# Optimization experiments

Hardware: AMD Instinct MI355X
Metric: run time of the kernel (lower is better)

The kernel has to match this reference:

```python
import jax, jax.numpy as jnp
import numpy as np

DIM = 1024
NUM_HEADS = 16
HEAD_DIM = DIM // NUM_HEADS


def _slopes(num_heads):
    ratio = 2.0 ** (-8.0 / num_heads)
    return jnp.asarray([ratio ** i for i in range(1, num_heads + 1)], dtype=jnp.float32)


def setup_inputs() -> dict:
    key = jax.random.key(0)
    ks = jax.random.split(key, 10)
    b, q_len, k_len = 2, 2048, 4096
    query = jax.random.normal(ks[0], (b, q_len, DIM), dtype=jnp.float32)
    keys = jax.random.normal(ks[1], (b, k_len, DIM), dtype=jnp.float32)
    values = jax.random.normal(ks[2], (b, k_len, DIM), dtype=jnp.float32)
    query_pos = jnp.sort(jax.random.randint(ks[3], (b, q_len), 0, 8192), axis=-1)
    key_pos = jnp.sort(jax.random.randint(ks[4], (b, k_len), 0, 8192), axis=-1)
    mask = jnp.ones((b, q_len, k_len), dtype=jnp.int32)
    # xavier-uniform-like linear weights, torch layout [out, in]
    lim = float(np.sqrt(6.0 / (DIM + DIM)))
    W_q = jax.random.uniform(ks[5], (DIM, DIM), minval=-lim, maxval=lim, dtype=jnp.float32)
    W_k = jax.random.uniform(ks[6], (DIM, DIM), minval=-lim, maxval=lim, dtype=jnp.float32)
    W_v = jax.random.uniform(ks[7], (DIM, DIM), minval=-lim, maxval=lim, dtype=jnp.float32)
    W_o = jax.random.uniform(ks[8], (DIM, DIM), minval=-lim, maxval=lim, dtype=jnp.float32)
    return {"query": query, "keys": keys, "values": values,
            "W_q": W_q, "W_k": W_k, "W_v": W_v, "W_o": W_o,
            "query_pos": query_pos, "key_pos": key_pos, "mask": mask}


def reference(query, keys, values, W_q, W_k, W_v, W_o, query_pos, key_pos, mask):
    b, q_len, _ = query.shape
    k_len = keys.shape[1]
    scale = 1.0 / np.sqrt(HEAD_DIM)
    # project and split heads: [b, h, len, d]
    Q = (query @ W_q.T).reshape(b, q_len, NUM_HEADS, HEAD_DIM).transpose(0, 2, 1, 3)
    K = (keys @ W_k.T).reshape(b, k_len, NUM_HEADS, HEAD_DIM).transpose(0, 2, 1, 3)
    V = (values @ W_v.T).reshape(b, k_len, NUM_HEADS, HEAD_DIM).transpose(0, 2, 1, 3)
    scores = jnp.einsum('bhqd,bhkd->bhqk', Q, K) * scale
    # ALiBi bias: -slope_h * (q_pos - k_pos)
    dist = (query_pos[:, :, None] - key_pos[:, None, :]).astype(scores.dtype)  # [b,q,k]
    bias = -_slopes(NUM_HEADS)[None, :, None, None] * dist[:, None, :, :]
    scores = scores + bias
    scores = jnp.where(mask[:, None, :, :] == 0, -jnp.inf, scores)
    # softmax1 exactly as source: exp(x - max) / (1 + sum(exp(x - max)))
    m = jnp.max(scores, axis=-1, keepdims=True)
    e = jnp.exp(scores - m)
    attn = e / (1.0 + jnp.sum(e, axis=-1, keepdims=True))
    out = jnp.einsum('bhqk,bhkd->bhqd', attn, V)
    out = out.transpose(0, 2, 1, 3).reshape(b, q_len, DIM)
    return out @ W_o.T
```

## Files before the change

### kernel.cpp

```cpp
#include <hip/hip_runtime.h>


typedef short bf16x8 __attribute__((ext_vector_type(8)));
typedef short s16x4  __attribute__((ext_vector_type(4)));
typedef float f32x4  __attribute__((ext_vector_type(4)));

#define MFMA16(a,b,c) __builtin_amdgcn_mfma_f32_16x16x32_bf16(a,b,c,0,0,0)

__device__ __forceinline__ short f2bf(float x) {
  unsigned u = __float_as_uint(x);
  u = (u + 0x7fffu + ((u >> 16) & 1u)) >> 16;
  return (short)u;
}

__device__ __forceinline__ void gload16(const void* g, void* l) {
  __builtin_amdgcn_global_load_lds((const __attribute__((address_space(1))) void*)g,
                                   (__attribute__((address_space(3))) void*)l, 16, 0, 0);
}

__global__ __launch_bounds__(256) void convert_kernel(
    const float* __restrict__ q,  const float* __restrict__ k,  const float* __restrict__ v,
    const float* __restrict__ wq, const float* __restrict__ wk, const float* __restrict__ wv,
    const float* __restrict__ wo,
    short* __restrict__ qb, short* __restrict__ kb, short* __restrict__ vb,
    short* __restrict__ wqb, short* __restrict__ wkb, short* __restrict__ wvb,
    short* __restrict__ wob)
{
  long c = (long)blockIdx.x * 256 + threadIdx.x;
  const float QSCALE = 0.125f * 1.44269504088896f;
  const float* src; short* dst; long base; float scale = 1.0f;
  if      (c < 1048576) { src = q;  dst = qb;  base = 0;       }
  else if (c < 3145728) { src = k;  dst = kb;  base = 1048576; }
  else if (c < 5242880) { src = v;  dst = vb;  base = 3145728; }
  else if (c < 5505024) { src = wq; dst = wqb; base = 5242880; scale = QSCALE; }
  else if (c < 5767168) { src = wk; dst = wkb; base = 5505024; }
  else if (c < 6029312) { src = wv; dst = wvb; base = 5767168; }
  else                  { src = wo; dst = wob; base = 6029312; }
  long i = (c - base) * 4;
  float4 x = *(const float4*)(src + i);
  s16x4 o = { f2bf(x.x * scale), f2bf(x.y * scale), f2bf(x.z * scale), f2bf(x.w * scale) };
  *(s16x4*)(dst + i) = o;
}

template<int MODE>
__global__ __launch_bounds__(256) void gemm_bt(const short* __restrict__ A,
                                               const short* __restrict__ B,
                                               void* __restrict__ Cout)
{
  __shared__ alignas(16) short As[2][128 * 64];
  __shared__ alignas(16) short Bs[2][128 * 64];
  const int tid  = threadIdx.x;
  const int wave = tid >> 6, lane = tid & 63;
  const int lo = lane & 15, g = lane >> 4;
  const int wm = wave >> 1, wn = wave & 1;
  const int m0 = blockIdx.x * 128, n0 = blockIdx.y * 128;

  f32x4 acc[4][4];
  const f32x4 Z4 = {0.f, 0.f, 0.f, 0.f};
#pragma unroll
  for (int i = 0; i < 4; i++)
#pragma unroll
    for (int j = 0; j < 4; j++) acc[i][j] = Z4;

  auto stage = [&](int buf, int k0) {
#pragma unroll
    for (int i = 0; i < 4; i++) {
      int c = i * 256 + tid;
      gload16(A + (long)(m0 + (c >> 3)) * 1024 + k0 + (c & 7) * 8,
              &As[buf][(i * 256 + wave * 64) * 8]);
    }
#pragma unroll
    for (int i = 0; i < 4; i++) {
      int c = i * 256 + tid;
      gload16(B + (long)(n0 + (c >> 3)) * 1024 + k0 + (c & 7) * 8,
              &Bs[buf][(i * 256 + wave * 64) * 8]);
    }
  };

  stage(0, 0);
  __syncthreads();
  int cur = 0;
  for (int t = 0; t < 16; t++) {
    if (t < 15) stage(cur ^ 1, (t + 1) * 64);
#pragma unroll
    for (int kk = 0; kk < 2; kk++) {
      bf16x8 af[4], bfr[4];
#pragma unroll
      for (int mi = 0; mi < 4; mi++)
        af[mi] = *(const bf16x8*)&As[cur][(wm * 64 + mi * 16 + lo) * 64 + kk * 32 + g * 8];
#pragma unroll
      for (int ni = 0; ni < 4; ni++)
        bfr[ni] = *(const bf16x8*)&Bs[cur][(wn * 64 + ni * 16 + lo) * 64 + kk * 32 + g * 8];
#pragma unroll
      for (int mi = 0; mi < 4; mi++)
#pragma unroll
        for (int ni = 0; ni < 4; ni++)
          acc[mi][ni] = MFMA16(af[mi], bfr[ni], acc[mi][ni]);
    }
    __syncthreads();
    cur ^= 1;
  }

  const int rbase = m0 + wm * 64, cbase = n0 + wn * 64;
  if (MODE == 0 || MODE == 2) {
#pragma unroll
    for (int mi = 0; mi < 4; mi++)
#pragma unroll
      for (int ni = 0; ni < 4; ni++) {
        int row = rbase + mi * 16 + g * 4;
        int col = cbase + ni * 16 + lo;
#pragma unroll
        for (int r = 0; r < 4; r++) {
          if (MODE == 0) ((short*)Cout)[(long)(row + r) * 1024 + col] = f2bf(acc[mi][ni][r]);
          else           ((float*)Cout)[(long)(row + r) * 1024 + col] = acc[mi][ni][r];
        }
      }
  } else {
#pragma unroll
    for (int mi = 0; mi < 4; mi++)
#pragma unroll
      for (int ni = 0; ni < 4; ni++) {
        int mrow = rbase + mi * 16 + g * 4;
        int n    = cbase + ni * 16 + lo;
        int b    = mrow >> 12, key = mrow & 4095;
        s16x4 pk = { f2bf(acc[mi][ni][0]), f2bf(acc[mi][ni][1]),
                     f2bf(acc[mi][ni][2]), f2bf(acc[mi][ni][3]) };
        *(s16x4*)((short*)Cout + ((long)(b * 1024 + n)) * 4096 + key) = pk;
      }
  }
}

__global__ __launch_bounds__(256) void attn_kernel(
    const short* __restrict__ Qp, const short* __restrict__ Kp, const short* __restrict__ Vt,
    const int* __restrict__ qpos, const int* __restrict__ kpos, short* __restrict__ AO)
{
  __shared__ float skp_lds[4096];
  __shared__ alignas(16) short P_lds[4][32 * 72];
  const int tid = threadIdx.x;
  const int wv = tid >> 6, lane = tid & 63;
  const int lo = lane & 15, g = lane >> 4;
  const int qt = blockIdx.x, bh = blockIdx.y;
  const int b = bh >> 4, h = bh & 15;
  const float slope2 = exp2f(-0.5f * (float)(h + 1)) * 1.44269504088896f;

  for (int i = tid; i < 4096; i += 256)
    skp_lds[i] = slope2 * (float)kpos[b * 4096 + i];
  __syncthreads();

  const int  q0   = qt * 128 + wv * 32;
  const long qrow = (long)b * 2048 + q0;

  bf16x8 qf[2][2];
#pragma unroll
  for (int mi = 0; mi < 2; mi++)
#pragma unroll
    for (int kk = 0; kk < 2; kk++)
      qf[mi][kk] = *(const bf16x8*)(Qp + (qrow + mi * 16 + lo) * 1024 + h * 64 + kk * 32 + g * 8);

  float sqp[2][4];
#pragma unroll
  for (int mi = 0; mi < 2; mi++)
#pragma unroll
    for (int r = 0; r < 4; r++)
      sqp[mi][r] = slope2 * (float)qpos[qrow + mi * 16 + g * 4 + r];

  float m_[2][4], l_[2][4];
  f32x4 acc[2][4];
  const f32x4 Z4 = {0.f, 0.f, 0.f, 0.f};
#pragma unroll
  for (int mi = 0; mi < 2; mi++) {
#pragma unroll
    for (int r = 0; r < 4; r++) { m_[mi][r] = -__builtin_inff(); l_[mi][r] = 0.f; }
#pragma unroll
    for (int ni = 0; ni < 4; ni++) acc[mi][ni] = Z4;
  }

  short* Pw = &P_lds[wv][0];
  const short* Kb = Kp + (long)b * 4096 * 1024 + h * 64;
  const short* Vb = Vt + (long)bh * 64 * 4096;

  for (int kb = 0; kb < 4096; kb += 64) {
    bf16x8 kf[2][4];
#pragma unroll
    for (int kk = 0; kk < 2; kk++)
#pragma unroll
      for (int nk = 0; nk < 4; nk++)
        kf[kk][nk] = *(const bf16x8*)(Kb + (long)(kb + nk * 16 + lo) * 1024 + kk * 32 + g * 8);

    f32x4 S[2][4];
#pragma unroll
    for (int mi = 0; mi < 2; mi++)
#pragma unroll
      for (int nk = 0; nk < 4; nk++) S[mi][nk] = Z4;
#pragma unroll
    for (int mi = 0; mi < 2; mi++)
#pragma unroll
      for (int nk = 0; nk < 4; nk++)
#pragma unroll
        for (int kk = 0; kk < 2; kk++)
          S[mi][nk] = MFMA16(qf[mi][kk], kf[kk][nk], S[mi][nk]);

    float skp[4];
#pragma unroll
    for (int nk = 0; nk < 4; nk++) skp[nk] = skp_lds[kb + nk * 16 + lo];

#pragma unroll
    for (int mi = 0; mi < 2; mi++)
#pragma unroll
      for (int nk = 0; nk < 4; nk++)
#pragma unroll
        for (int r = 0; r < 4; r++)
          S[mi][nk][r] += skp[nk] - sqp[mi][r];

#pragma unroll
    for (int mi = 0; mi < 2; mi++)
#pragma unroll
      for (int r = 0; r < 4; r++) {
        float rm = fmaxf(fmaxf(S[mi][0][r], S[mi][1][r]), fmaxf(S[mi][2][r], S[mi][3][r]));
#pragma unroll
        for (int d = 1; d < 16; d <<= 1) rm = fmaxf(rm, __shfl_xor(rm, d));
        float mn = fmaxf(m_[mi][r], rm);
        float rf = exp2f(m_[mi][r] - mn);
        m_[mi][r] = mn;
        float rs = 0.f;
#pragma unroll
        for (int nk = 0; nk < 4; nk++) {
          float p = exp2f(S[mi][nk][r] - mn);
          rs += p;
          Pw[(mi * 16 + g * 4 + r) * 72 + nk * 16 + lo] = f2bf(p);
        }
        l_[mi][r] = l_[mi][r] * rf + rs;
#pragma unroll
        for (int ni = 0; ni < 4; ni++) acc[mi][ni][r] *= rf;
      }

    bf16x8 pa[2][2];
#pragma unroll
    for (int mi = 0; mi < 2; mi++)
#pragma unroll
      for (int k2 = 0; k2 < 2; k2++)
        pa[mi][k2] = *(const bf16x8*)(Pw + (mi * 16 + lo) * 72 + k2 * 32 + g * 8);
    bf16x8 vf[2][4];
#pragma unroll
    for (int k2 = 0; k2 < 2; k2++)
#pragma unroll
      for (int ni = 0; ni < 4; ni++)
        vf[k2][ni] = *(const bf16x8*)(Vb + (long)(ni * 16 + lo) * 4096 + kb + k2 * 32 + g * 8);
#pragma unroll
    for (int mi = 0; mi < 2; mi++)
#pragma unroll
      for (int ni = 0; ni < 4; ni++)
#pragma unroll
        for (int k2 = 0; k2 < 2; k2++)
          acc[mi][ni] = MFMA16(pa[mi][k2], vf[k2][ni], acc[mi][ni]);
  }

#pragma unroll
  for (int mi = 0; mi < 2; mi++)
#pragma unroll
    for (int r = 0; r < 4; r++) {
      float ls = l_[mi][r];
#pragma unroll
      for (int d = 1; d < 16; d <<= 1) ls += __shfl_xor(ls, d);
      float inv = 1.0f / (1.0f + ls);
      long row = qrow + mi * 16 + g * 4 + r;
#pragma unroll
      for (int ni = 0; ni < 4; ni++)
        AO[row * 1024 + h * 64 + ni * 16 + lo] = f2bf(acc[mi][ni][r] * inv);
    }
}

extern "C" void kernel_launch(void* const* d_in, const int* in_sizes, int n_in,
                              void* d_out, int out_size, void* d_ws, size_t ws_size,
                              hipStream_t stream)
{
  const float* q  = (const float*)d_in[0];
  const float* k  = (const float*)d_in[1];
  const float* v  = (const float*)d_in[2];
  const float* wq = (const float*)d_in[3];
  const float* wk = (const float*)d_in[4];
  const float* wv = (const float*)d_in[5];
  const float* wo = (const float*)d_in[6];
  const int* qpos = (const int*)d_in[7];
  const int* kpos = (const int*)d_in[8];

  char* ws = (char*)d_ws;
  const size_t MB = 1u << 20;
  short* qbf = (short*)(ws + 0  * MB);
  short* kbf = (short*)(ws + 8  * MB);
  short* vbf = (short*)(ws + 24 * MB);
  short* wqb = (short*)(ws + 40 * MB);
  short* wkb = (short*)(ws + 42 * MB);
  short* wvb = (short*)(ws + 44 * MB);
  short* wob = (short*)(ws + 46 * MB);
  short* Qp  = (short*)(ws + 48 * MB);
  short* Kp  = (short*)(ws + 56 * MB);
  short* Vt  = (short*)(ws + 72 * MB);
  short* AO  = (short*)(ws + 88 * MB);

  convert_kernel<<<24576, 256, 0, stream>>>(q, k, v, wq, wk, wv, wo,
                                            qbf, kbf, vbf, wqb, wkb, wvb, wob);
  gemm_bt<0><<<dim3(32, 8), 256, 0, stream>>>(qbf, wqb, Qp);
  gemm_bt<0><<<dim3(64, 8), 256, 0, stream>>>(kbf, wkb, Kp);
  gemm_bt<1><<<dim3(64, 8), 256, 0, stream>>>(vbf, wvb, Vt);
  attn_kernel<<<dim3(16, 32), 256, 0, stream>>>(Qp, Kp, Vt, qpos, kpos, AO);
  gemm_bt<2><<<dim3(32, 8), 256, 0, stream>>>(AO, wob, d_out);
}
```

Before: 564.7 us.

## Shrink attention query tile, drop query-position bias, retile small GEMMs

The attention kernel now gives each wave 16 query rows instead of 32 and launches twice as many blocks, ordered head-major, with a launch-bounds occupancy hint. It drops the per-row query-position ALiBi term, since that term is constant along each softmax row and cancels. P is written transposed with packed bf16 conversion instructions and read back element-wise into MFMA operands. The Q and output projection GEMMs use a 64-row tile so they launch more blocks. The smaller query tile means each K/V load serves fewer rows, which raises global traffic per unit of work.

```diff
diff --git a/kernel.cpp b/kernel.cpp
--- a/kernel.cpp
+++ b/kernel.cpp
@@ -11,6 +11,12 @@
   unsigned u = __float_as_uint(x);
   u = (u + 0x7fffu + ((u >> 16) & 1u)) >> 16;
   return (short)u;
+}
+
+__device__ __forceinline__ unsigned cvt_pk_bf16(float a, float b) {
+  unsigned r;
+  asm("v_cvt_pk_bf16_f32 %0, %1, %2" : "=v"(r) : "v"(a), "v"(b));
+  return r;
 }
 
 __device__ __forceinline__ void gload16(const void* g, void* l) {
@@ -42,29 +48,33 @@
   *(s16x4*)(dst + i) = o;
 }
 
-template<int MODE>
+template<int MODE, int BM>
 __global__ __launch_bounds__(256) void gemm_bt(const short* __restrict__ A,
                                                const short* __restrict__ B,
                                                void* __restrict__ Cout)
 {
-  __shared__ alignas(16) short As[2][128 * 64];
+  constexpr int WCOLS = (BM == 128) ? 2 : 4;
+  constexpr int TN    = 128 / WCOLS;
+  constexpr int NI    = TN / 16;
+  constexpr int APASS = BM / 32;
+  __shared__ alignas(16) short As[2][BM * 64];
   __shared__ alignas(16) short Bs[2][128 * 64];
   const int tid  = threadIdx.x;
   const int wave = tid >> 6, lane = tid & 63;
   const int lo = lane & 15, g = lane >> 4;
-  const int wm = wave >> 1, wn = wave & 1;
-  const int m0 = blockIdx.x * 128, n0 = blockIdx.y * 128;
-
-  f32x4 acc[4][4];
+  const int wm = wave / WCOLS, wn = wave % WCOLS;
+  const int m0 = blockIdx.x * BM, n0 = blockIdx.y * 128;
+
+  f32x4 acc[4][NI];
   const f32x4 Z4 = {0.f, 0.f, 0.f, 0.f};
 #pragma unroll
   for (int i = 0; i < 4; i++)
 #pragma unroll
-    for (int j = 0; j < 4; j++) acc[i][j] = Z4;
+    for (int j = 0; j < NI; j++) acc[i][j] = Z4;
 
   auto stage = [&](int buf, int k0) {
 #pragma unroll
-    for (int i = 0; i < 4; i++) {
+    for (int i = 0; i < APASS; i++) {
       int c = i * 256 + tid;
       gload16(A + (long)(m0 + (c >> 3)) * 1024 + k0 + (c & 7) * 8,
               &As[buf][(i * 256 + wave * 64) * 8]);
@@ -84,29 +94,29 @@
     if (t < 15) stage(cur ^ 1, (t + 1) * 64);
 #pragma unroll
     for (int kk = 0; kk < 2; kk++) {
-      bf16x8 af[4], bfr[4];
+      bf16x8 af[4], bfr[NI];
 #pragma unroll
       for (int mi = 0; mi < 4; mi++)
         af[mi] = *(const bf16x8*)&As[cur][(wm * 64 + mi * 16 + lo) * 64 + kk * 32 + g * 8];
 #pragma unroll
-      for (int ni = 0; ni < 4; ni++)
-        bfr[ni] = *(const bf16x8*)&Bs[cur][(wn * 64 + ni * 16 + lo) * 64 + kk * 32 + g * 8];
+      for (int ni = 0; ni < NI; ni++)
+        bfr[ni] = *(const bf16x8*)&Bs[cur][(wn * TN + ni * 16 + lo) * 64 + kk * 32 + g * 8];
 #pragma unroll
       for (int mi = 0; mi < 4; mi++)
 #pragma unroll
-        for (int ni = 0; ni < 4; ni++)
+        for (int ni = 0; ni < NI; ni++)
           acc[mi][ni] = MFMA16(af[mi], bfr[ni], acc[mi][ni]);
     }
     __syncthreads();
     cur ^= 1;
   }
 
-  const int rbase = m0 + wm * 64, cbase = n0 + wn * 64;
+  const int rbase = m0 + wm * 64, cbase = n0 + wn * TN;
   if (MODE == 0 || MODE == 2) {
 #pragma unroll
     for (int mi = 0; mi < 4; mi++)
 #pragma unroll
-      for (int ni = 0; ni < 4; ni++) {
+      for (int ni = 0; ni < NI; ni++) {
         int row = rbase + mi * 16 + g * 4;
         int col = cbase + ni * 16 + lo;
 #pragma unroll
@@ -119,7 +129,7 @@
 #pragma unroll
     for (int mi = 0; mi < 4; mi++)
 #pragma unroll
-      for (int ni = 0; ni < 4; ni++) {
+      for (int ni = 0; ni < NI; ni++) {
         int mrow = rbase + mi * 16 + g * 4;
         int n    = cbase + ni * 16 + lo;
         int b    = mrow >> 12, key = mrow & 4095;
@@ -130,16 +140,16 @@
   }
 }
 
-__global__ __launch_bounds__(256) void attn_kernel(
+__global__ __launch_bounds__(256, 4) void attn_kernel(
     const short* __restrict__ Qp, const short* __restrict__ Kp, const short* __restrict__ Vt,
-    const int* __restrict__ qpos, const int* __restrict__ kpos, short* __restrict__ AO)
+    const int* __restrict__ kpos, short* __restrict__ AO)
 {
   __shared__ float skp_lds[4096];
-  __shared__ alignas(16) short P_lds[4][32 * 72];
+  __shared__ alignas(16) short P_lds[4][64 * 20];
   const int tid = threadIdx.x;
   const int wv = tid >> 6, lane = tid & 63;
   const int lo = lane & 15, g = lane >> 4;
-  const int qt = blockIdx.x, bh = blockIdx.y;
+  const int bh = blockIdx.x, qt = blockIdx.y;
   const int b = bh >> 4, h = bh & 15;
   const float slope2 = exp2f(-0.5f * (float)(h + 1)) * 1.44269504088896f;
 
@@ -147,33 +157,20 @@
     skp_lds[i] = slope2 * (float)kpos[b * 4096 + i];
   __syncthreads();
 
-  const int  q0   = qt * 128 + wv * 32;
-  const long qrow = (long)b * 2048 + q0;
-
-  bf16x8 qf[2][2];
-#pragma unroll
-  for (int mi = 0; mi < 2; mi++)
-#pragma unroll
-    for (int kk = 0; kk < 2; kk++)
-      qf[mi][kk] = *(const bf16x8*)(Qp + (qrow + mi * 16 + lo) * 1024 + h * 64 + kk * 32 + g * 8);
-
-  float sqp[2][4];
-#pragma unroll
-  for (int mi = 0; mi < 2; mi++)
-#pragma unroll
-    for (int r = 0; r < 4; r++)
-      sqp[mi][r] = slope2 * (float)qpos[qrow + mi * 16 + g * 4 + r];
-
-  float m_[2][4], l_[2][4];
-  f32x4 acc[2][4];
+  const long qrow = (long)b * 2048 + qt * 64 + wv * 16;
+
+  bf16x8 qf[2];
+#pragma unroll
+  for (int kk = 0; kk < 2; kk++)
+    qf[kk] = *(const bf16x8*)(Qp + (qrow + lo) * 1024 + h * 64 + kk * 32 + g * 8);
+
+  float m_[4], l_[4];
+  f32x4 acc[4];
   const f32x4 Z4 = {0.f, 0.f, 0.f, 0.f};
 #pragma unroll
-  for (int mi = 0; mi < 2; mi++) {
-#pragma unroll
-    for (int r = 0; r < 4; r++) { m_[mi][r] = -__builtin_inff(); l_[mi][r] = 0.f; }
-#pragma unroll
-    for (int ni = 0; ni < 4; ni++) acc[mi][ni] = Z4;
-  }
+  for (int r = 0; r < 4; r++) { m_[r] = -__builtin_inff(); l_[r] = 0.f; }
+#pragma unroll
+  for (int ni = 0; ni < 4; ni++) acc[ni] = Z4;
 
   short* Pw = &P_lds[wv][0];
   const short* Kb = Kp + (long)b * 4096 * 1024 + h * 64;
@@ -187,59 +184,63 @@
       for (int nk = 0; nk < 4; nk++)
         kf[kk][nk] = *(const bf16x8*)(Kb + (long)(kb + nk * 16 + lo) * 1024 + kk * 32 + g * 8);
 
-    f32x4 S[2][4];
-#pragma unroll
-    for (int mi = 0; mi < 2; mi++)
-#pragma unroll
-      for (int nk = 0; nk < 4; nk++) S[mi][nk] = Z4;
-#pragma unroll
-    for (int mi = 0; mi < 2; mi++)
-#pragma unroll
-      for (int nk = 0; nk < 4; nk++)
-#pragma unroll
-        for (int kk = 0; kk < 2; kk++)
-          S[mi][nk] = MFMA16(qf[mi][kk], kf[kk][nk], S[mi][nk]);
+    f32x4 S[4];
+#pragma unroll
+    for (int nk = 0; nk < 4; nk++) S[nk] = Z4;
+#pragma unroll
+    for (int nk = 0; nk < 4; nk++)
+#pragma unroll
+      for (int kk = 0; kk < 2; kk++)
+        S[nk] = MFMA16(qf[kk], kf[kk][nk], S[nk]);
 
     float skp[4];
 #pragma unroll
     for (int nk = 0; nk < 4; nk++) skp[nk] = skp_lds[kb + nk * 16 + lo];
-
-#pragma unroll
-    for (int mi = 0; mi < 2; mi++)
-#pragma unroll
-      for (int nk = 0; nk < 4; nk++)
-#pragma unroll
-        for (int r = 0; r < 4; r++)
-          S[mi][nk][r] += skp[nk] - sqp[mi][r];
-
-#pragma unroll
-    for (int mi = 0; mi < 2; mi++)
-#pragma unroll
-      for (int r = 0; r < 4; r++) {
-        float rm = fmaxf(fmaxf(S[mi][0][r], S[mi][1][r]), fmaxf(S[mi][2][r], S[mi][3][r]));
-#pragma unroll
-        for (int d = 1; d < 16; d <<= 1) rm = fmaxf(rm, __shfl_xor(rm, d));
-        float mn = fmaxf(m_[mi][r], rm);
-        float rf = exp2f(m_[mi][r] - mn);
-        m_[mi][r] = mn;
-        float rs = 0.f;
-#pragma unroll
-        for (int nk = 0; nk < 4; nk++) {
-          float p = exp2f(S[mi][nk][r] - mn);
-          rs += p;
-          Pw[(mi * 16 + g * 4 + r) * 72 + nk * 16 + lo] = f2bf(p);
-        }
-        l_[mi][r] = l_[mi][r] * rf + rs;
-#pragma unroll
-        for (int ni = 0; ni < 4; ni++) acc[mi][ni][r] *= rf;
-      }
-
-    bf16x8 pa[2][2];
-#pragma unroll
-    for (int mi = 0; mi < 2; mi++)
-#pragma unroll
-      for (int k2 = 0; k2 < 2; k2++)
-        pa[mi][k2] = *(const bf16x8*)(Pw + (mi * 16 + lo) * 72 + k2 * 32 + g * 8);
+#pragma unroll
+    for (int nk = 0; nk < 4; nk++)
+#pragma unroll
+      for (int r = 0; r < 4; r++) S[nk][r] += skp[nk];
+
+    float mn[4], rf[4];
+#pragma unroll
+    for (int r = 0; r < 4; r++) {
+      float rm = fmaxf(fmaxf(S[0][r], S[1][r]), fmaxf(S[2][r], S[3][r]));
+#pragma unroll
+      for (int d = 1; d < 16; d <<= 1) rm = fmaxf(rm, __shfl_xor(rm, d));
+      mn[r] = fmaxf(m_[r], rm);
+      rf[r] = exp2f(m_[r] - mn[r]);
+      m_[r] = mn[r];
+    }
+
+    float rs0 = 0.f, rs1 = 0.f, rs2 = 0.f, rs3 = 0.f;
+#pragma unroll
+    for (int nk = 0; nk < 4; nk++) {
+      float p0 = exp2f(S[nk][0] - mn[0]);
+      float p1 = exp2f(S[nk][1] - mn[1]);
+      float p2 = exp2f(S[nk][2] - mn[2]);
+      float p3 = exp2f(S[nk][3] - mn[3]);
+      rs0 += p0; rs1 += p1; rs2 += p2; rs3 += p3;
+      uint2 w = { cvt_pk_bf16(p0, p1), cvt_pk_bf16(p2, p3) };
+      *(uint2*)(Pw + (nk * 16 + lo) * 20 + g * 4) = w;
+    }
+    l_[0] = l_[0] * rf[0] + rs0;
+    l_[1] = l_[1] * rf[1] + rs1;
+    l_[2] = l_[2] * rf[2] + rs2;
+    l_[3] = l_[3] * rf[3] + rs3;
+#pragma unroll
+    for (int ni = 0; ni < 4; ni++)
+#pragma unroll
+      for (int r = 0; r < 4; r++) acc[ni][r] *= rf[r];
+
+    bf16x8 pa[2];
+#pragma unroll
+    for (int k2 = 0; k2 < 2; k2++) {
+      bf16x8 t;
+#pragma unroll
+      for (int j = 0; j < 8; j++)
+        t[j] = Pw[(k2 * 32 + g * 8 + j) * 20 + lo];
+      pa[k2] = t;
+    }
     bf16x8 vf[2][4];
 #pragma unroll
     for (int k2 = 0; k2 < 2; k2++)
@@ -247,27 +248,23 @@
       for (int ni = 0; ni < 4; ni++)
         vf[k2][ni] = *(const bf16x8*)(Vb + (long)(ni * 16 + lo) * 4096 + kb + k2 * 32 + g * 8);
 #pragma unroll
-    for (int mi = 0; mi < 2; mi++)
-#pragma unroll
-      for (int ni = 0; ni < 4; ni++)
-#pragma unroll
-        for (int k2 = 0; k2 < 2; k2++)
-          acc[mi][ni] = MFMA16(pa[mi][k2], vf[k2][ni], acc[mi][ni]);
+    for (int ni = 0; ni < 4; ni++)
+#pragma unroll
+      for (int k2 = 0; k2 < 2; k2++)
+        acc[ni] = MFMA16(pa[k2], vf[k2][ni], acc[ni]);
   }
 
 #pragma unroll
-  for (int mi = 0; mi < 2; mi++)
-#pragma unroll
-    for (int r = 0; r < 4; r++) {
-      float ls = l_[mi][r];
-#pragma unroll
-      for (int d = 1; d < 16; d <<= 1) ls += __shfl_xor(ls, d);
-      float inv = 1.0f / (1.0f + ls);
-      long row = qrow + mi * 16 + g * 4 + r;
-#pragma unroll
-      for (int ni = 0; ni < 4; ni++)
-        AO[row * 1024 + h * 64 + ni * 16 + lo] = f2bf(acc[mi][ni][r] * inv);
-    }
+  for (int r = 0; r < 4; r++) {
+    float ls = l_[r];
+#pragma unroll
+    for (int d = 1; d < 16; d <<= 1) ls += __shfl_xor(ls, d);
+    float inv = 1.0f / (1.0f + ls);
+    long row = qrow + g * 4 + r;
+#pragma unroll
+    for (int ni = 0; ni < 4; ni++)
+      AO[row * 1024 + h * 64 + ni * 16 + lo] = f2bf(acc[ni][r] * inv);
+  }
 }
 
 extern "C" void kernel_launch(void* const* d_in, const int* in_sizes, int n_in,
@@ -281,7 +278,6 @@
   const float* wk = (const float*)d_in[4];
   const float* wv = (const float*)d_in[5];
   const float* wo = (const float*)d_in[6];
-  const int* qpos = (const int*)d_in[7];
   const int* kpos = (const int*)d_in[8];
 
   char* ws = (char*)d_ws;
@@ -300,9 +296,9 @@
 
   convert_kernel<<<24576, 256, 0, stream>>>(q, k, v, wq, wk, wv, wo,
                                             qbf, kbf, vbf, wqb, wkb, wvb, wob);
-  gemm_bt<0><<<dim3(32, 8), 256, 0, stream>>>(qbf, wqb, Qp);
-  gemm_bt<0><<<dim3(64, 8), 256, 0, stream>>>(kbf, wkb, Kp);
-  gemm_bt<1><<<dim3(64, 8), 256, 0, stream>>>(vbf, wvb, Vt);
-  attn_kernel<<<dim3(16, 32), 256, 0, stream>>>(Qp, Kp, Vt, qpos, kpos, AO);
-  gemm_bt<2><<<dim3(32, 8), 256, 0, stream>>>(AO, wob, d_out);
-}
+  gemm_bt<0, 64> <<<dim3(64, 8), 256, 0, stream>>>(qbf, wqb, Qp);
+  gemm_bt<0, 128><<<dim3(64, 8), 256, 0, stream>>>(kbf, wkb, Kp);
+  gemm_bt<1, 128><<<dim3(64, 8), 256, 0, stream>>>(vbf, wvb, Vt);
+  attn_kernel<<<dim3(32, 32), 256, 0, stream>>>(Qp, Kp, Vt, kpos, AO);
+  gemm_bt<2, 64> <<<dim3(64, 8), 256, 0, stream>>>(AO, wob, d_out);
+}
```

New measurement: 733.7 us. 29.9% more time.
